# Performance work log

Hardware: AMD Instinct MI355X
Metric: run time of the kernel (lower is better)

The kernel has to match this reference:

```python
import jax, jax.numpy as jnp
import numpy as np

N = 20000
IN_C = 512
HID = 64
H1 = 8
OUT_C = 256
E = 320000
NEG_SLOPE = 0.2


def gat_conv(x, src, dst, W, a_src, a_dst, b, concat):
    # PyG GATConv (shared lin for src/dst), inference mode (no dropout).
    H, C = a_src.shape
    h = (x @ W).reshape(N, H, C)                      # [N,H,C]
    alpha_src = (h * a_src[None]).sum(-1)             # [N,H]
    alpha_dst = (h * a_dst[None]).sum(-1)             # [N,H]
    alpha = jax.nn.leaky_relu(alpha_src[src] + alpha_dst[dst], NEG_SLOPE)  # [E,H]
    # segment softmax over incoming edges of each dst node
    amax = jax.ops.segment_max(alpha, dst, num_segments=N)
    amax = jnp.where(jnp.isfinite(amax), amax, 0.0)
    ex = jnp.exp(alpha - amax[dst])
    denom = jax.ops.segment_sum(ex, dst, num_segments=N)
    coef = ex / (denom[dst] + 1e-16)                  # [E,H]
    msg = h[src] * coef[:, :, None]                   # [E,H,C]
    out = jax.ops.segment_sum(msg, dst, num_segments=N)  # [N,H,C]
    out = out.reshape(N, H * C) if concat else out.mean(axis=1)
    return out + b


def setup_inputs() -> dict:
    key = jax.random.key(0)
    ks = jax.random.split(key, 10)
    x = jax.random.normal(ks[0], (N, IN_C), dtype=jnp.float32)
    edge_index = jax.random.randint(ks[1], (2, E), 0, N, dtype=jnp.int32)
    s1 = 1.0 / np.sqrt(IN_C)
    s2 = 1.0 / np.sqrt(HID * H1)
    W1 = jax.random.uniform(ks[2], (IN_C, H1 * HID), jnp.float32, -s1, s1)
    att_src1 = jax.random.uniform(ks[3], (H1, HID), jnp.float32, -s1, s1)
    att_dst1 = jax.random.uniform(ks[4], (H1, HID), jnp.float32, -s1, s1)
    b1 = jnp.zeros((H1 * HID,), jnp.float32)
    W2 = jax.random.uniform(ks[5], (H1 * HID, OUT_C), jnp.float32, -s2, s2)
    att_src2 = jax.random.uniform(ks[6], (1, OUT_C), jnp.float32, -s2, s2)
    att_dst2 = jax.random.uniform(ks[7], (1, OUT_C), jnp.float32, -s2, s2)
    b2 = jnp.zeros((OUT_C,), jnp.float32)
    return {"x": x, "edge_index": edge_index, "W1": W1, "att_src1": att_src1,
            "att_dst1": att_dst1, "b1": b1, "W2": W2, "att_src2": att_src2,
            "att_dst2": att_dst2, "b2": b2}


def reference(x, edge_index, W1, att_src1, att_dst1, b1, W2, att_src2, att_dst2, b2):
    # add self-loops (PyG GATConv default add_self_loops=True)
    loop = jnp.arange(N, dtype=edge_index.dtype)
    src = jnp.concatenate([edge_index[0], loop])
    dst = jnp.concatenate([edge_index[1], loop])
    h = gat_conv(x, src, dst, W1, att_src1, att_dst1, b1, concat=True)
    h = jax.nn.elu(h)
    out = gat_conv(h, src, dst, W2, att_src2, att_dst2, b2, concat=False)
    return jax.nn.log_softmax(out, axis=1)
```

## Files before the change

### kernel.cpp

```cpp
#include <hip/hip_runtime.h>
#include <math.h>

#define N_NODES 20000
#define IN_CH   512
#define HID_TOT 512
#define OUT_CH  256
#define N_EDGE  320000
#define TOT_EDGE (N_EDGE + N_NODES)

typedef __attribute__((ext_vector_type(8))) short short8;
typedef __attribute__((ext_vector_type(4))) float f32x4;
typedef __attribute__((ext_vector_type(2))) float f32x2;

__device__ __forceinline__ ushort f2bf(float f) {
    union { float f; unsigned u; } v; v.f = f;
    unsigned u = v.u;
    return (ushort)((u + 0x7fffu + ((u >> 16) & 1u)) >> 16);
}
__device__ __forceinline__ float bf2f(ushort u) {
    union { unsigned u; float f; } v; v.u = ((unsigned)u) << 16; return v.f;
}

__device__ __forceinline__ void glds16(const ushort* g, ushort* l) {
    __builtin_amdgcn_global_load_lds(
        (const __attribute__((address_space(1))) void*)g,
        (__attribute__((address_space(3))) void*)l, 16, 0, 0);
}

__device__ __forceinline__ float lrelu(float a) { return fmaxf(a, 0.2f * a); }

#define NA_BLK (N_NODES * IN_CH / 4 / 256)
#define NB_BLK ((IN_CH / 64) * (HID_TOT / 4))
#define NC_BLK ((HID_TOT / 64) * (OUT_CH / 4))
#define NZ_BLK ((N_NODES + 255) / 256)
__global__ __launch_bounds__(256) void prep_kernel(const float* __restrict__ x,
                                                   ushort* __restrict__ xb,
                                                   const float* __restrict__ W1,
                                                   ushort* __restrict__ w1t,
                                                   const float* __restrict__ W2,
                                                   ushort* __restrict__ w2t,
                                                   int* __restrict__ counts,
                                                   float* __restrict__ as2,
                                                   float* __restrict__ ad2) {
    int b = blockIdx.x;
    int t = threadIdx.x;
    if (b < NA_BLK) {
        int i = b * 256 + t;
        float4 v = *(const float4*)&x[(size_t)i * 4];
        ushort4 o = make_ushort4(f2bf(v.x), f2bf(v.y), f2bf(v.z), f2bf(v.w));
        *(ushort4*)&xb[(size_t)i * 4] = o;
    } else if (b < NA_BLK + NB_BLK) {
        int bb = b - NA_BLK;
        int k = (bb & 7) * 64 + (t & 63);
        int n = (bb >> 3) * 4 + (t >> 6);
        w1t[(size_t)n * IN_CH + k] = f2bf(W1[(size_t)k * HID_TOT + n]);
    } else if (b < NA_BLK + NB_BLK + NC_BLK) {
        int bb = b - NA_BLK - NB_BLK;
        int k = (bb & 7) * 64 + (t & 63);
        int n = (bb >> 3) * 4 + (t >> 6);
        w2t[(size_t)n * HID_TOT + k] = f2bf(W2[(size_t)k * OUT_CH + n]);
    } else {
        int i = (b - NA_BLK - NB_BLK - NC_BLK) * 256 + t;
        if (i < N_NODES) { counts[i] = 0; as2[i] = 0.f; ad2[i] = 0.f; }
    }
}

__global__ void hist_kernel(const int* __restrict__ ei, int* __restrict__ counts) {
    int e = blockIdx.x * blockDim.x + threadIdx.x;
    if (e >= TOT_EDGE) return;
    int d = (e < N_EDGE) ? ei[N_EDGE + e] : (e - N_EDGE);
    atomicAdd(&counts[d], 1);
}

__global__ __launch_bounds__(1024) void scan_kernel(const int* __restrict__ counts,
                                                    int* __restrict__ offsets,
                                                    int* __restrict__ cursors) {
    const int C = (N_NODES + 1023) / 1024;
    int t = threadIdx.x;
    int lane = t & 63, wid = t >> 6;
    int base = t * C;
    int sum = 0;
#pragma unroll
    for (int i = 0; i < C; i++) {
        int idx = base + i;
        if (idx < N_NODES) sum += counts[idx];
    }
    int val = sum;
#pragma unroll
    for (int off = 1; off < 64; off <<= 1) {
        int y = __shfl_up(val, off);
        if (lane >= off) val += y;
    }
    __shared__ int wsum[16], woff[16], stotal;
    if (lane == 63) wsum[wid] = val;
    __syncthreads();
    if (t == 0) {
        int r = 0;
        for (int w = 0; w < 16; w++) { woff[w] = r; r += wsum[w]; }
        stotal = r;
    }
    __syncthreads();
    int running = woff[wid] + (val - sum);
#pragma unroll
    for (int i = 0; i < C; i++) {
        int idx = base + i;
        if (idx < N_NODES) {
            offsets[idx] = running;
            cursors[idx] = running;
            running += counts[idx];
        }
    }
    if (t == 0) offsets[N_NODES] = stotal;
}

__global__ void scatter_kernel(const int* __restrict__ ei, int* __restrict__ cursors,
                               int* __restrict__ srcs) {
    int e = blockIdx.x * blockDim.x + threadIdx.x;
    if (e >= TOT_EDGE) return;
    int s, d;
    if (e < N_EDGE) { s = ei[e]; d = ei[N_EDGE + e]; } else { s = e - N_EDGE; d = s; }
    int pos = atomicAdd(&cursors[d], 1);
    srcs[pos] = s;
}

__global__ __launch_bounds__(256) void gemm_mfma_kernel(const ushort* __restrict__ A,
                                                        const ushort* __restrict__ Bt,
                                                        unsigned char* __restrict__ Cf8,
                                                        const float* __restrict__ asrc,
                                                        const float* __restrict__ adst,
                                                        float* __restrict__ as_out,
                                                        float* __restrict__ ad_out,
                                                        int M, int N, int K, int layer1) {
    __shared__ ushort As[128 * 32];
    __shared__ ushort Bs[128 * 32];
    int t = threadIdx.x;
    int lane = t & 63;
    int wave = t >> 6;
    int wm = (wave >> 1) * 64, wn = (wave & 1) * 64;
    int bm = blockIdx.y * 128, bn = blockIdx.x * 128;
    int q = lane >> 4, l15 = lane & 15;

    int c0 = t, c1 = t + 256;
    int r0 = c0 >> 2, kq0 = (c0 & 3) * 8;
    int r1 = c1 >> 2, kq1 = (c1 & 3) * 8;
    int ar0 = bm + r0; if (ar0 >= M) ar0 = M - 1;
    int ar1 = bm + r1; if (ar1 >= M) ar1 = M - 1;
    const ushort* A0 = A + (size_t)ar0 * K + kq0;
    const ushort* A1 = A + (size_t)ar1 * K + kq1;
    const ushort* B0 = Bt + (size_t)(bn + r0) * K + kq0;
    const ushort* B1 = Bt + (size_t)(bn + r1) * K + kq1;
    ushort* As0 = &As[r0 * 32 + kq0];
    ushort* As1 = &As[r1 * 32 + kq1];
    ushort* Bs0 = &Bs[r0 * 32 + kq0];
    ushort* Bs1 = &Bs[r1 * 32 + kq1];

    f32x4 acc[4][4];
#pragma unroll
    for (int i = 0; i < 4; i++)
#pragma unroll
        for (int j = 0; j < 4; j++) acc[i][j] = f32x4{0.f, 0.f, 0.f, 0.f};

    for (int k0 = 0; k0 < K; k0 += 32) {
        __syncthreads();
        glds16(A0 + k0, As0);
        glds16(A1 + k0, As1);
        glds16(B0 + k0, Bs0);
        glds16(B1 + k0, Bs1);
        __syncthreads();

        short8 af[4], bf[4];
#pragma unroll
        for (int i = 0; i < 4; i++)
            af[i] = *(const short8*)&As[(wm + i * 16 + l15) * 32 + q * 8];
#pragma unroll
        for (int j = 0; j < 4; j++)
            bf[j] = *(const short8*)&Bs[(wn + j * 16 + l15) * 32 + q * 8];
#pragma unroll
        for (int i = 0; i < 4; i++)
#pragma unroll
            for (int j = 0; j < 4; j++)
                acc[i][j] = __builtin_amdgcn_mfma_f32_16x16x32_bf16(af[i], bf[j], acc[i][j], 0, 0, 0);
    }

    int colbase = bn + wn;
    float av[4], dv[4];
#pragma unroll
    for (int j = 0; j < 4; j++) {
        int cg = colbase + j * 16 + l15;
        av[j] = asrc[cg];
        dv[j] = adst[cg];
    }
    float ps[4][4], pd[4][4];
#pragma unroll
    for (int i = 0; i < 4; i++)
#pragma unroll
        for (int r = 0; r < 4; r++) {
            float p = 0.f, d = 0.f;
#pragma unroll
            for (int j = 0; j < 4; j++) {
                p = fmaf(acc[i][j][r], av[j], p);
                d = fmaf(acc[i][j][r], dv[j], d);
            }
            ps[i][r] = p; pd[i][r] = d;
        }
#pragma unroll
    for (int off = 1; off < 16; off <<= 1) {
#pragma unroll
        for (int i = 0; i < 4; i++)
#pragma unroll
            for (int r = 0; r < 4; r++) {
                ps[i][r] += __shfl_xor(ps[i][r], off);
                pd[i][r] += __shfl_xor(pd[i][r], off);
            }
    }

    int hidx = colbase >> 6;
#pragma unroll
    for (int i = 0; i < 4; i++) {
#pragma unroll
        for (int r = 0; r < 4; r++) {
            int rg = bm + wm + i * 16 + q * 4 + r;
            if (rg < M) {
#pragma unroll
                for (int j = 0; j < 4; j++) {
                    int cg = colbase + j * 16 + l15;
                    int w8 = __builtin_amdgcn_cvt_pk_fp8_f32(acc[i][j][r], acc[i][j][r], 0, false);
                    Cf8[(size_t)rg * N + cg] = (unsigned char)(w8 & 0xff);
                }
                if (l15 == 0) {
                    if (layer1) {
                        as_out[rg * 8 + hidx] = ps[i][r];
                        ad_out[rg * 8 + hidx] = pd[i][r];
                    } else {
                        atomicAdd(&as_out[rg], ps[i][r]);
                        atomicAdd(&ad_out[rg], pd[i][r]);
                    }
                }
            }
        }
    }
}

__global__ __launch_bounds__(64) void agg1_kernel(const unsigned char* __restrict__ h1f,
                                                  const float* __restrict__ as1,
                                                  const float* __restrict__ ad1,
                                                  const int* __restrict__ offsets,
                                                  const int* __restrict__ srcs,
                                                  const float* __restrict__ b1,
                                                  ushort* __restrict__ h1ab) {
    int v = blockIdx.x;
    int t = threadIdx.x;
    int h = t >> 3;
    int c8 = t << 3;
    int s = offsets[v], e = offsets[v + 1];
    float adv = ad1[v * 8 + h];

    float denom = 0.f;
    float acc[8];
#pragma unroll
    for (int k = 0; k < 8; k++) acc[k] = 0.f;

    int i = s;
    for (; i + 8 <= e; i += 8) {
        int sn[8];
#pragma unroll
        for (int j = 0; j < 8; j++) sn[j] = srcs[i + j];
        uint2 r[8];
#pragma unroll
        for (int j = 0; j < 8; j++)
            r[j] = *(const uint2*)&h1f[(size_t)sn[j] * HID_TOT + c8];
        float w[8];
#pragma unroll
        for (int j = 0; j < 8; j++) {
            float a = lrelu(as1[sn[j] * 8 + h] + adv);
            w[j] = __expf(a);
            denom += w[j];
        }
#pragma unroll
        for (int j = 0; j < 8; j++) {
            f32x2 pa = __builtin_amdgcn_cvt_pk_f32_fp8(r[j].x, false);
            f32x2 pb = __builtin_amdgcn_cvt_pk_f32_fp8(r[j].x, true);
            f32x2 pc = __builtin_amdgcn_cvt_pk_f32_fp8(r[j].y, false);
            f32x2 pdd = __builtin_amdgcn_cvt_pk_f32_fp8(r[j].y, true);
            acc[0] = fmaf(w[j], pa.x, acc[0]); acc[1] = fmaf(w[j], pa.y, acc[1]);
            acc[2] = fmaf(w[j], pb.x, acc[2]); acc[3] = fmaf(w[j], pb.y, acc[3]);
            acc[4] = fmaf(w[j], pc.x, acc[4]); acc[5] = fmaf(w[j], pc.y, acc[5]);
            acc[6] = fmaf(w[j], pdd.x, acc[6]); acc[7] = fmaf(w[j], pdd.y, acc[7]);
        }
    }
    for (; i + 4 <= e; i += 4) {
        int sn[4];
#pragma unroll
        for (int j = 0; j < 4; j++) sn[j] = srcs[i + j];
        uint2 r[4];
#pragma unroll
        for (int j = 0; j < 4; j++)
            r[j] = *(const uint2*)&h1f[(size_t)sn[j] * HID_TOT + c8];
#pragma unroll
        for (int j = 0; j < 4; j++) {
            float a = lrelu(as1[sn[j] * 8 + h] + adv);
            float w = __expf(a);
            denom += w;
            f32x2 pa = __builtin_amdgcn_cvt_pk_f32_fp8(r[j].x, false);
            f32x2 pb = __builtin_amdgcn_cvt_pk_f32_fp8(r[j].x, true);
            f32x2 pc = __builtin_amdgcn_cvt_pk_f32_fp8(r[j].y, false);
            f32x2 pdd = __builtin_amdgcn_cvt_pk_f32_fp8(r[j].y, true);
            acc[0] = fmaf(w, pa.x, acc[0]); acc[1] = fmaf(w, pa.y, acc[1]);
            acc[2] = fmaf(w, pb.x, acc[2]); acc[3] = fmaf(w, pb.y, acc[3]);
            acc[4] = fmaf(w, pc.x, acc[4]); acc[5] = fmaf(w, pc.y, acc[5]);
            acc[6] = fmaf(w, pdd.x, acc[6]); acc[7] = fmaf(w, pdd.y, acc[7]);
        }
    }
    for (; i < e; i++) {
        int sn = srcs[i];
        uint2 r = *(const uint2*)&h1f[(size_t)sn * HID_TOT + c8];
        float a = lrelu(as1[sn * 8 + h] + adv);
        float w = __expf(a);
        denom += w;
        f32x2 pa = __builtin_amdgcn_cvt_pk_f32_fp8(r.x, false);
        f32x2 pb = __builtin_amdgcn_cvt_pk_f32_fp8(r.x, true);
        f32x2 pc = __builtin_amdgcn_cvt_pk_f32_fp8(r.y, false);
        f32x2 pdd = __builtin_amdgcn_cvt_pk_f32_fp8(r.y, true);
        acc[0] = fmaf(w, pa.x, acc[0]); acc[1] = fmaf(w, pa.y, acc[1]);
        acc[2] = fmaf(w, pb.x, acc[2]); acc[3] = fmaf(w, pb.y, acc[3]);
        acc[4] = fmaf(w, pc.x, acc[4]); acc[5] = fmaf(w, pc.y, acc[5]);
        acc[6] = fmaf(w, pdd.x, acc[6]); acc[7] = fmaf(w, pdd.y, acc[7]);
    }

    float inv = 1.f / (denom + 1e-16f);
    short8 ov;
#pragma unroll
    for (int k = 0; k < 8; k++) {
        float o = acc[k] * inv + b1[c8 + k];
        o = (o > 0.f) ? o : expm1f(o);
        ov[k] = (short)f2bf(o);
    }
    *(short8*)&h1ab[(size_t)v * HID_TOT + c8] = ov;
}

__global__ __launch_bounds__(64) void agg2_kernel(const unsigned char* __restrict__ h2f,
                                                  const float* __restrict__ as2,
                                                  const float* __restrict__ ad2,
                                                  const int* __restrict__ offsets,
                                                  const int* __restrict__ srcs,
                                                  const float* __restrict__ b2,
                                                  float* __restrict__ out) {
    int v = blockIdx.x;
    int t = threadIdx.x;
    int c4 = t << 2;
    int s = offsets[v], e = offsets[v + 1];
    float adv = ad2[v];

    float denom = 0.f;
    float acc[4];
#pragma unroll
    for (int k = 0; k < 4; k++) acc[k] = 0.f;

    int i = s;
    for (; i + 8 <= e; i += 8) {
        int sn[8];
#pragma unroll
        for (int j = 0; j < 8; j++) sn[j] = srcs[i + j];
        unsigned u[8];
#pragma unroll
        for (int j = 0; j < 8; j++)
            u[j] = *(const unsigned*)&h2f[(size_t)sn[j] * OUT_CH + c4];
        float w[8];
#pragma unroll
        for (int j = 0; j < 8; j++) {
            float a = lrelu(as2[sn[j]] + adv);
            w[j] = __expf(a);
            denom += w[j];
        }
#pragma unroll
        for (int j = 0; j < 8; j++) {
            f32x2 pa = __builtin_amdgcn_cvt_pk_f32_fp8(u[j], false);
            f32x2 pb = __builtin_amdgcn_cvt_pk_f32_fp8(u[j], true);
            acc[0] = fmaf(w[j], pa.x, acc[0]); acc[1] = fmaf(w[j], pa.y, acc[1]);
            acc[2] = fmaf(w[j], pb.x, acc[2]); acc[3] = fmaf(w[j], pb.y, acc[3]);
        }
    }
    for (; i + 4 <= e; i += 4) {
        int sn[4];
#pragma unroll
        for (int j = 0; j < 4; j++) sn[j] = srcs[i + j];
        unsigned u[4];
#pragma unroll
        for (int j = 0; j < 4; j++)
            u[j] = *(const unsigned*)&h2f[(size_t)sn[j] * OUT_CH + c4];
#pragma unroll
        for (int j = 0; j < 4; j++) {
            float a = lrelu(as2[sn[j]] + adv);
            float w = __expf(a);
            denom += w;
            f32x2 pa = __builtin_amdgcn_cvt_pk_f32_fp8(u[j], false);
            f32x2 pb = __builtin_amdgcn_cvt_pk_f32_fp8(u[j], true);
            acc[0] = fmaf(w, pa.x, acc[0]); acc[1] = fmaf(w, pa.y, acc[1]);
            acc[2] = fmaf(w, pb.x, acc[2]); acc[3] = fmaf(w, pb.y, acc[3]);
        }
    }
    for (; i < e; i++) {
        int sn = srcs[i];
        unsigned u = *(const unsigned*)&h2f[(size_t)sn * OUT_CH + c4];
        float a = lrelu(as2[sn] + adv);
        float w = __expf(a);
        denom += w;
        f32x2 pa = __builtin_amdgcn_cvt_pk_f32_fp8(u, false);
        f32x2 pb = __builtin_amdgcn_cvt_pk_f32_fp8(u, true);
        acc[0] = fmaf(w, pa.x, acc[0]); acc[1] = fmaf(w, pa.y, acc[1]);
        acc[2] = fmaf(w, pb.x, acc[2]); acc[3] = fmaf(w, pb.y, acc[3]);
    }

    float inv = 1.f / (denom + 1e-16f);
    float4 bb = *(const float4*)&b2[c4];
    float4 x;
    x.x = acc[0] * inv + bb.x; x.y = acc[1] * inv + bb.y;
    x.z = acc[2] * inv + bb.z; x.w = acc[3] * inv + bb.w;

    float mm = fmaxf(fmaxf(x.x, x.y), fmaxf(x.z, x.w));
#pragma unroll
    for (int off = 1; off < 64; off <<= 1) mm = fmaxf(mm, __shfl_xor(mm, off));
    float sum = __expf(x.x - mm) + __expf(x.y - mm) + __expf(x.z - mm) + __expf(x.w - mm);
#pragma unroll
    for (int off = 1; off < 64; off <<= 1) sum += __shfl_xor(sum, off);
    float ls = logf(sum);
    float4 o;
    o.x = x.x - mm - ls; o.y = x.y - mm - ls; o.z = x.z - mm - ls; o.w = x.w - mm - ls;
    *(float4*)&out[(size_t)v * OUT_CH + c4] = o;
}

static inline size_t align256(size_t x) { return (x + 255) & ~(size_t)255; }

extern "C" void kernel_launch(void* const* d_in, const int* in_sizes, int n_in,
                              void* d_out, int out_size, void* d_ws, size_t ws_size,
                              hipStream_t stream) {
    const float* x    = (const float*)d_in[0];
    const int*   ei   = (const int*)d_in[1];
    const float* W1   = (const float*)d_in[2];
    const float* as1w = (const float*)d_in[3];
    const float* ad1w = (const float*)d_in[4];
    const float* b1   = (const float*)d_in[5];
    const float* W2   = (const float*)d_in[6];
    const float* as2w = (const float*)d_in[7];
    const float* ad2w = (const float*)d_in[8];
    const float* b2   = (const float*)d_in[9];
    float* out = (float*)d_out;

    char* p = (char*)d_ws;
    unsigned char* h1f = (unsigned char*)p; p += align256((size_t)N_NODES * HID_TOT);
    unsigned char* h2f = (unsigned char*)p; p += align256((size_t)N_NODES * OUT_CH);
    ushort* xb   = (ushort*)p; p += align256(sizeof(ushort) * (size_t)N_NODES * IN_CH);
    ushort* h1ab = xb;
    ushort* w1t  = (ushort*)p; p += align256(sizeof(ushort) * (size_t)IN_CH * HID_TOT);
    ushort* w2t  = (ushort*)p; p += align256(sizeof(ushort) * (size_t)HID_TOT * OUT_CH);
    float* as1  = (float*)p; p += align256(sizeof(float) * (size_t)N_NODES * 8);
    float* ad1  = (float*)p; p += align256(sizeof(float) * (size_t)N_NODES * 8);
    float* as2  = (float*)p; p += align256(sizeof(float) * (size_t)N_NODES);
    float* ad2  = (float*)p; p += align256(sizeof(float) * (size_t)N_NODES);
    int* counts  = (int*)p; p += align256(sizeof(int) * (size_t)N_NODES);
    int* offsets = (int*)p; p += align256(sizeof(int) * (size_t)(N_NODES + 1));
    int* cursors = (int*)p; p += align256(sizeof(int) * (size_t)N_NODES);
    int* srcs    = (int*)p; p += align256(sizeof(int) * (size_t)TOT_EDGE);

    prep_kernel<<<NA_BLK + NB_BLK + NC_BLK + NZ_BLK, 256, 0, stream>>>(
        x, xb, W1, w1t, W2, w2t, counts, as2, ad2);

    int eb = (TOT_EDGE + 255) / 256;
    hist_kernel<<<eb, 256, 0, stream>>>(ei, counts);
    scan_kernel<<<1, 1024, 0, stream>>>(counts, offsets, cursors);
    scatter_kernel<<<eb, 256, 0, stream>>>(ei, cursors, srcs);

    gemm_mfma_kernel<<<dim3(HID_TOT / 128, (N_NODES + 127) / 128), 256, 0, stream>>>(
        xb, w1t, h1f, as1w, ad1w, as1, ad1, N_NODES, HID_TOT, IN_CH, 1);
    agg1_kernel<<<N_NODES, 64, 0, stream>>>(h1f, as1, ad1, offsets, srcs, b1, h1ab);

    gemm_mfma_kernel<<<dim3(OUT_CH / 128, (N_NODES + 127) / 128), 256, 0, stream>>>(
        h1ab, w2t, h2f, as2w, ad2w, as2, ad2, N_NODES, OUT_CH, HID_TOT, 0);
    agg2_kernel<<<N_NODES, 64, 0, stream>>>(h2f, as2, ad2, offsets, srcs, b2, out);
}
```

Measured before the change: 282.0 us.

## Retile GEMM to 128x64 blocks with K=64 and XOR-swizzled LDS

Changes the MFMA GEMM block tile from 128x128 with K-step 32 to 128x64 with K-step 64. Each wave now owns a 32x64 slab, and the LDS layout is XOR-swizzled to avoid bank conflicts on the short8 reads. This doubles the grid size for better CU occupancy on the small-N GEMMs and halves the number of K-loop barriers. In exchange, each block reuses its A tile across fewer columns, and the attention-logit head index now comes straight from blockIdx.x, which relies on 64-wide column tiles.

```diff
diff --git a/kernel.cpp b/kernel.cpp
--- a/kernel.cpp
+++ b/kernel.cpp
@@ -16,9 +16,6 @@
     union { float f; unsigned u; } v; v.f = f;
     unsigned u = v.u;
     return (ushort)((u + 0x7fffu + ((u >> 16) & 1u)) >> 16);
-}
-__device__ __forceinline__ float bf2f(ushort u) {
-    union { unsigned u; float f; } v; v.u = ((unsigned)u) << 16; return v.f;
 }
 
 __device__ __forceinline__ void glds16(const ushort* g, ushort* l) {
@@ -131,68 +128,85 @@
                                                         float* __restrict__ as_out,
                                                         float* __restrict__ ad_out,
                                                         int M, int N, int K, int layer1) {
-    __shared__ ushort As[128 * 32];
-    __shared__ ushort Bs[128 * 32];
+    __shared__ ushort As[128 * 64];
+    __shared__ ushort Bs[64 * 64];
     int t = threadIdx.x;
     int lane = t & 63;
     int wave = t >> 6;
-    int wm = (wave >> 1) * 64, wn = (wave & 1) * 64;
-    int bm = blockIdx.y * 128, bn = blockIdx.x * 128;
+    int wm = wave * 32;
+    int bm = blockIdx.y * 128, bn = blockIdx.x * 64;
     int q = lane >> 4, l15 = lane & 15;
 
-    int c0 = t, c1 = t + 256;
-    int r0 = c0 >> 2, kq0 = (c0 & 3) * 8;
-    int r1 = c1 >> 2, kq1 = (c1 & 3) * 8;
-    int ar0 = bm + r0; if (ar0 >= M) ar0 = M - 1;
-    int ar1 = bm + r1; if (ar1 >= M) ar1 = M - 1;
-    const ushort* A0 = A + (size_t)ar0 * K + kq0;
-    const ushort* A1 = A + (size_t)ar1 * K + kq1;
-    const ushort* B0 = Bt + (size_t)(bn + r0) * K + kq0;
-    const ushort* B1 = Bt + (size_t)(bn + r1) * K + kq1;
-    ushort* As0 = &As[r0 * 32 + kq0];
-    ushort* As1 = &As[r1 * 32 + kq1];
-    ushort* Bs0 = &Bs[r0 * 32 + kq0];
-    ushort* Bs1 = &Bs[r1 * 32 + kq1];
-
-    f32x4 acc[4][4];
-#pragma unroll
-    for (int i = 0; i < 4; i++)
+    const ushort* Aptr[4]; ushort* Alds[4];
+    const ushort* Bptr[2]; ushort* Blds[2];
+#pragma unroll
+    for (int k = 0; k < 4; k++) {
+        int c = t + 256 * k;
+        int r = c >> 3, kqs = c & 7;
+        int kqg = kqs ^ (r & 7);
+        int ar = bm + r; if (ar >= M) ar = M - 1;
+        Aptr[k] = A + (size_t)ar * K + kqg * 8;
+        Alds[k] = &As[c * 8];
+    }
+#pragma unroll
+    for (int k = 0; k < 2; k++) {
+        int c = t + 256 * k;
+        int r = c >> 3, kqs = c & 7;
+        int kqg = kqs ^ (r & 7);
+        Bptr[k] = Bt + (size_t)(bn + r) * K + kqg * 8;
+        Blds[k] = &Bs[c * 8];
+    }
+
+    f32x4 acc[2][4];
+#pragma unroll
+    for (int i = 0; i < 2; i++)
 #pragma unroll
         for (int j = 0; j < 4; j++) acc[i][j] = f32x4{0.f, 0.f, 0.f, 0.f};
 
-    for (int k0 = 0; k0 < K; k0 += 32) {
+    for (int k0 = 0; k0 < K; k0 += 64) {
         __syncthreads();
-        glds16(A0 + k0, As0);
-        glds16(A1 + k0, As1);
-        glds16(B0 + k0, Bs0);
-        glds16(B1 + k0, Bs1);
+        glds16(Aptr[0] + k0, Alds[0]);
+        glds16(Aptr[1] + k0, Alds[1]);
+        glds16(Aptr[2] + k0, Alds[2]);
+        glds16(Aptr[3] + k0, Alds[3]);
+        glds16(Bptr[0] + k0, Blds[0]);
+        glds16(Bptr[1] + k0, Blds[1]);
         __syncthreads();
 
-        short8 af[4], bf[4];
-#pragma unroll
-        for (int i = 0; i < 4; i++)
-            af[i] = *(const short8*)&As[(wm + i * 16 + l15) * 32 + q * 8];
-#pragma unroll
-        for (int j = 0; j < 4; j++)
-            bf[j] = *(const short8*)&Bs[(wn + j * 16 + l15) * 32 + q * 8];
-#pragma unroll
-        for (int i = 0; i < 4; i++)
-#pragma unroll
-            for (int j = 0; j < 4; j++)
-                acc[i][j] = __builtin_amdgcn_mfma_f32_16x16x32_bf16(af[i], bf[j], acc[i][j], 0, 0, 0);
-    }
-
-    int colbase = bn + wn;
+#pragma unroll
+        for (int s = 0; s < 2; s++) {
+            int kq = s * 4 + q;
+            short8 af[2], bf[4];
+#pragma unroll
+            for (int i = 0; i < 2; i++) {
+                int row = wm + i * 16 + l15;
+                int slot = kq ^ (row & 7);
+                af[i] = *(const short8*)&As[row * 64 + slot * 8];
+            }
+#pragma unroll
+            for (int j = 0; j < 4; j++) {
+                int row = j * 16 + l15;
+                int slot = kq ^ (row & 7);
+                bf[j] = *(const short8*)&Bs[row * 64 + slot * 8];
+            }
+#pragma unroll
+            for (int i = 0; i < 2; i++)
+#pragma unroll
+                for (int j = 0; j < 4; j++)
+                    acc[i][j] = __builtin_amdgcn_mfma_f32_16x16x32_bf16(af[i], bf[j], acc[i][j], 0, 0, 0);
+        }
+    }
+
     float av[4], dv[4];
 #pragma unroll
     for (int j = 0; j < 4; j++) {
-        int cg = colbase + j * 16 + l15;
+        int cg = bn + j * 16 + l15;
         av[j] = asrc[cg];
         dv[j] = adst[cg];
     }
-    float ps[4][4], pd[4][4];
-#pragma unroll
-    for (int i = 0; i < 4; i++)
+    float ps[2][4], pd[2][4];
+#pragma unroll
+    for (int i = 0; i < 2; i++)
 #pragma unroll
         for (int r = 0; r < 4; r++) {
             float p = 0.f, d = 0.f;
@@ -206,7 +220,7 @@
 #pragma unroll
     for (int off = 1; off < 16; off <<= 1) {
 #pragma unroll
-        for (int i = 0; i < 4; i++)
+        for (int i = 0; i < 2; i++)
 #pragma unroll
             for (int r = 0; r < 4; r++) {
                 ps[i][r] += __shfl_xor(ps[i][r], off);
@@ -214,16 +228,16 @@
             }
     }
 
-    int hidx = colbase >> 6;
-#pragma unroll
-    for (int i = 0; i < 4; i++) {
+    int hidx = blockIdx.x;
+#pragma unroll
+    for (int i = 0; i < 2; i++) {
 #pragma unroll
         for (int r = 0; r < 4; r++) {
             int rg = bm + wm + i * 16 + q * 4 + r;
             if (rg < M) {
 #pragma unroll
                 for (int j = 0; j < 4; j++) {
-                    int cg = colbase + j * 16 + l15;
+                    int cg = bn + j * 16 + l15;
                     int w8 = __builtin_amdgcn_cvt_pk_fp8_f32(acc[i][j][r], acc[i][j][r], 0, false);
                     Cf8[(size_t)rg * N + cg] = (unsigned char)(w8 & 0xff);
                 }
@@ -470,11 +484,11 @@
     scan_kernel<<<1, 1024, 0, stream>>>(counts, offsets, cursors);
     scatter_kernel<<<eb, 256, 0, stream>>>(ei, cursors, srcs);
 
-    gemm_mfma_kernel<<<dim3(HID_TOT / 128, (N_NODES + 127) / 128), 256, 0, stream>>>(
+    gemm_mfma_kernel<<<dim3(HID_TOT / 64, (N_NODES + 127) / 128), 256, 0, stream>>>(
         xb, w1t, h1f, as1w, ad1w, as1, ad1, N_NODES, HID_TOT, IN_CH, 1);
     agg1_kernel<<<N_NODES, 64, 0, stream>>>(h1f, as1, ad1, offsets, srcs, b1, h1ab);
 
-    gemm_mfma_kernel<<<dim3(OUT_CH / 128, (N_NODES + 127) / 128), 256, 0, stream>>>(
+    gemm_mfma_kernel<<<dim3(OUT_CH / 64, (N_NODES + 127) / 128), 256, 0, stream>>>(
         h1ab, w2t, h2f, as2w, ad2w, as2, ad2, N_NODES, OUT_CH, HID_TOT, 0);
     agg2_kernel<<<N_NODES, 64, 0, stream>>>(h2f, as2, ad2, offsets, srcs, b2, out);
 }
```

After: 275.7 us, median of 2. -2.2%, faster.
